# Kernel tuning notes

Measured on AMD Instinct MI355X. Metric: run time of the kernel, lower is better.

The kernel has to match this reference:

```python
import jax, jax.numpy as jnp
import numpy as np

B, C, H, W = 8, 512, 32, 32


def setup_inputs() -> dict:
    key = jax.random.key(0)
    ks = jax.random.split(key, 7)
    s = 0.02  # typical conv init scale
    return {
        "x": jax.random.normal(ks[0], (B, C, H, W), dtype=jnp.float32),
        "Wq": jax.random.normal(ks[1], (C, C), dtype=jnp.float32) * s,
        "bq": jax.random.normal(ks[2], (C,), dtype=jnp.float32) * s,
        "Wk": jax.random.normal(ks[3], (C, C), dtype=jnp.float32) * s,
        "bk": jax.random.normal(ks[4], (C,), dtype=jnp.float32) * s,
        "W6": jax.random.normal(ks[5], (C, C), dtype=jnp.float32) * s,
        "b6": jax.random.normal(ks[6], (C,), dtype=jnp.float32) * s,
    }


def _gam(x, Wq, bq, Wk, bk, W6, b6):
    b, c, h, w = x.shape
    hw = h * w
    scale = 1.0 / (c ** 0.5)
    # 1x1 convs == per-pixel channel matmuls (torch conv weight [out,in,1,1])
    q = jnp.einsum('bchw,dc->bhwd', x, Wq) + bq          # [B,H,W,C]
    q = q.reshape(b * hw, c)                              # query rows
    k = jnp.einsum('bchw,dc->bdhw', x, Wk) + bk[None, :, None, None]
    k = jnp.transpose(k, (1, 0, 2, 3)).reshape(c, b * hw)  # [C, B*HW]
    xw = (q.astype(jnp.float32) @ k.astype(jnp.float32))   # [B*HW, B*HW]
    xw = xw.reshape(b * hw, b, hw)
    xw = jnp.max(xw, axis=-1)                              # max over keys' spatial dim
    xw = jnp.mean(xw, axis=-1)                             # mean over key images
    xw = xw.reshape(b, hw) * scale
    xw = jax.nn.softmax(xw, axis=-1).astype(x.dtype)
    xw = xw.reshape(b, 1, h, w)
    x5 = x * xw
    return jnp.einsum('bchw,dc->bdhw', x5, W6) + b6[None, :, None, None]


def reference(x, Wq, bq, Wk, bk, W6, b6):
    x_new = _gam(x, Wq, bq, Wk, bk, W6, b6)
    # prototype: mean over batch and spatial dims, keep channels
    x_proto = jnp.mean(x_new.astype(jnp.float32), axis=(0, 2, 3)).astype(x.dtype)
    return x * x_proto[None, :, None, None]
```

## Files before the change

### kernel.cpp

```cpp
#include <hip/hip_runtime.h>
#include <hip/hip_bf16.h>

typedef __bf16 bf16_t;
typedef __bf16 bf16x8 __attribute__((ext_vector_type(8)));
typedef float f32x4 __attribute__((ext_vector_type(4)));

#define B_   8
#define C_   512
#define HW_  1024
#define NPIX 8192

typedef __attribute__((address_space(3))) void lds_vp;
typedef const __attribute__((address_space(1))) void gbl_vp;
__device__ __forceinline__ void gload_lds16(const void* g, void* l) {
    __builtin_amdgcn_global_load_lds((gbl_vp*)g, (lds_vp*)l, 16, 0, 0);
}

__device__ __forceinline__ void stage128x64_swz(const bf16_t* __restrict__ g,
                                                bf16_t* lds, int tid) {
    int w64 = tid & ~63;
#pragma unroll
    for (int s = 0; s < 4; ++s) {
        int u = s * 256 + tid;
        int row = u >> 3;
        int kg = (u & 7) ^ (row & 7);
        const bf16_t* src = g + (size_t)row * 512 + kg * 8;
        gload_lds16((const void*)src, (void*)(lds + (size_t)(s * 256 + w64) * 8));
    }
}

__global__ void k_transpose(const float* __restrict__ x, bf16_t* __restrict__ xT,
                            const float* __restrict__ Wq, const float* __restrict__ Wk,
                            bf16_t* __restrict__ wq, bf16_t* __restrict__ wk) {
    __shared__ bf16_t tile[64 * 66];
    int p0 = blockIdx.x * 64, c0 = blockIdx.y * 64, b = blockIdx.z;
    int t = threadIdx.x;
    int widx = ((blockIdx.z * 8 + blockIdx.y) * 16 + blockIdx.x) * 256 + t;
    wq[widx] = (bf16_t)Wq[widx];
    wk[widx] = (bf16_t)Wk[widx];
#pragma unroll
    for (int s = 0; s < 16; ++s) {
        int u = s * 256 + t;
        int cr = u >> 6, pc = u & 63;
        tile[cr * 66 + pc] = (bf16_t)x[((size_t)(b * C_ + c0 + cr)) * HW_ + p0 + pc];
    }
    __syncthreads();
#pragma unroll
    for (int s = 0; s < 16; ++s) {
        int u = s * 256 + t;
        int pr = u >> 6, cc = u & 63;
        xT[((size_t)(b * HW_ + p0 + pr)) * C_ + c0 + cc] = tile[cc * 66 + pr];
    }
}

__launch_bounds__(256, 2)
__global__ void k_gemm_qk(const bf16_t* __restrict__ xT,
                          const bf16_t* __restrict__ wq, const bf16_t* __restrict__ wk,
                          const float* __restrict__ bq, const float* __restrict__ bk,
                          bf16_t* __restrict__ qo, bf16_t* __restrict__ ko) {
    __shared__ __align__(16) bf16_t As[128 * 64];
    __shared__ __align__(16) bf16_t Bs[128 * 64];
    int bid = blockIdx.x;
    int mtile = bid >> 3;
    int nt = bid & 7;
    const bf16_t* wsel = (nt < 4) ? wq : wk;
    const float*  bsel = (nt < 4) ? bq : bk;
    bf16_t*       osel = (nt < 4) ? qo : ko;
    int nb = (nt & 3) * 128;
    int i0 = mtile * 128;
    int tid = threadIdx.x;
    int lane = tid & 63, w = tid >> 6;
    int wr = w >> 1, wc = w & 1, lr = lane & 15, lg = lane >> 4;
    int kswz = (lg ^ (lr & 7)) << 4;

    f32x4 acc[4][4];
#pragma unroll
    for (int mi = 0; mi < 4; ++mi)
#pragma unroll
        for (int ni = 0; ni < 4; ++ni)
#pragma unroll
            for (int r = 0; r < 4; ++r) acc[mi][ni][r] = 0.f;

    for (int kt = 0; kt < 8; ++kt) {
        int k0 = kt * 64;
        stage128x64_swz(xT + (size_t)i0 * 512 + k0, As, tid);
        stage128x64_swz(wsel + (size_t)nb * 512 + k0, Bs, tid);
        asm volatile("s_waitcnt vmcnt(0)" ::: "memory");
        __builtin_amdgcn_s_barrier();
#pragma unroll
        for (int kk = 0; kk < 2; ++kk) {
            bf16x8 af[4], bfr[4];
#pragma unroll
            for (int mi = 0; mi < 4; ++mi)
                af[mi] = *(const bf16x8*)((const char*)As +
                    (wr * 64 + mi * 16 + lr) * 128 + (kswz ^ (kk * 64)));
#pragma unroll
            for (int ni = 0; ni < 4; ++ni)
                bfr[ni] = *(const bf16x8*)((const char*)Bs +
                    (wc * 64 + ni * 16 + lr) * 128 + (kswz ^ (kk * 64)));
#pragma unroll
            for (int mi = 0; mi < 4; ++mi)
#pragma unroll
                for (int ni = 0; ni < 4; ++ni)
                    acc[mi][ni] = __builtin_amdgcn_mfma_f32_16x16x32_bf16(
                        af[mi], bfr[ni], acc[mi][ni], 0, 0, 0);
        }
        __builtin_amdgcn_s_barrier();
    }
#pragma unroll
    for (int ni = 0; ni < 4; ++ni) {
        int col = nb + wc * 64 + ni * 16 + lr;
        float bias = bsel[col];
#pragma unroll
        for (int mi = 0; mi < 4; ++mi) {
            int rowb = i0 + wr * 64 + mi * 16 + lg * 4;
#pragma unroll
            for (int r = 0; r < 4; ++r)
                osel[(size_t)(rowb + r) * 512 + col] = (bf16_t)(acc[mi][ni][r] + bias);
        }
    }
}


#define STAGE_A(RH, D, T)                                                          \
    gload_lds16((const void*)(q + srcA + (size_t)((RH) * 128) * 512 +              \
                              ((T) & 7) * 64),                                     \
                (void*)(ldsb + (RH) * 32768 + (D) * 16384 + ldw));                 \
    gload_lds16((const void*)(q + srcA + (size_t)((RH) * 128 + 64) * 512 +         \
                              ((T) & 7) * 64),                                     \
                (void*)(ldsb + (RH) * 32768 + (D) * 16384 + 8192 + ldw));

#define STAGE_B(RH, D, T)                                                          \
    gload_lds16((const void*)(kb + srcB +                                          \
                              (size_t)(((T) >> 3) * 256 + (RH) * 128) * 512 +      \
                              ((T) & 7) * 64),                                     \
                (void*)(ldsb + 65536 + (RH) * 32768 + (D) * 16384 + ldw));         \
    gload_lds16((const void*)(kb + srcB +                                          \
                              (size_t)(((T) >> 3) * 256 + (RH) * 128 + 64) * 512 + \
                              ((T) & 7) * 64),                                     \
                (void*)(ldsb + 65536 + (RH) * 32768 + (D) * 16384 + 8192 + ldw));

#define PHASE(D, KH, MH, STAGE_STMT, VM_STMT)                                      \
    {                                                                              \
        const char* Ab = ldsb + wr * 32768 + (D) * 16384;                          \
        const char* Bb = ldsb + 65536 + (wc >> 1) * 32768 + (D) * 16384;           \
        _Pragma("unroll")                                                          \
        for (int mi = 0; mi < 4; ++mi)                                             \
            af[mi] = *(const bf16x8*)(Ab + (aswz ^ ((KH) * 64)) +                  \
                                      ((MH) * 4 + mi) * 2048);                     \
        if ((MH) == 0) {                                                           \
            _Pragma("unroll")                                                      \
            for (int ni = 0; ni < 4; ++ni)                                         \
                bf[ni] = *(const bf16x8*)(Bb + (bswz ^ ((KH) * 64)) + ni * 2048);  \
        }                                                                          \
        STAGE_STMT;                                                                \
        __builtin_amdgcn_s_setprio(1);                                             \
        _Pragma("unroll")                                                          \
        for (int mi = 0; mi < 4; ++mi)                                             \
            _Pragma("unroll")                                                      \
            for (int ni = 0; ni < 4; ++ni)                                         \
                acc[(MH) * 4 + mi][ni] = __builtin_amdgcn_mfma_f32_16x16x32_bf16(  \
                    af[mi], bf[ni], acc[(MH) * 4 + mi][ni], 0, 0, 0);              \
        __builtin_amdgcn_s_setprio(0);                                             \
        VM_STMT;                                                                   \
        __builtin_amdgcn_s_barrier();                                              \
    }

__global__ __launch_bounds__(512, 2)
void k_gemm_max8(const bf16_t* __restrict__ q, const bf16_t* __restrict__ kp,
                 float* __restrict__ Mout) {
    __shared__ __align__(16) bf16_t lds[65536];
    char* ldsb = (char*)lds;
    int bid = blockIdx.x;
    int img = bid & 7;
    int qp = bid >> 3;
    int i0 = qp * 256;
    const bf16_t* kb = kp + (size_t)img * HW_ * C_;
    int tid = threadIdx.x;
    int lane = tid & 63, w = tid >> 6;
    int wr = w >> 2, wc = w & 3;
    int lr = lane & 15, lg = lane >> 4;
    int kswz = (lg ^ (lr & 7)) << 4;
    int aswz = lr * 128 + kswz;
    int bswz = ((wc & 1) * 64 + lr) * 128 + kswz;

    int srow = tid >> 3;
    int sk = (((tid & 7) ^ ((tid >> 3) & 7))) << 3;
    size_t srcA = (size_t)(i0 + srow) * 512 + sk;
    size_t srcB = (size_t)srow * 512 + sk;
    int ldw = (tid >> 6) * 1024;

    f32x4 acc[8][4];
    bf16x8 af[4], bf[4];
    float rm[8][4];
#pragma unroll
    for (int mi = 0; mi < 8; ++mi)
#pragma unroll
        for (int ni = 0; ni < 4; ++ni)
#pragma unroll
            for (int r = 0; r < 4; ++r) acc[mi][ni][r] = 0.f;
#pragma unroll
    for (int mi = 0; mi < 8; ++mi)
#pragma unroll
        for (int r = 0; r < 4; ++r) rm[mi][r] = -3.4e38f;

    STAGE_B(0, 0, 0) STAGE_A(0, 0, 0) STAGE_B(1, 0, 0) STAGE_A(1, 0, 0)
    STAGE_B(0, 1, 1)
    asm volatile("s_waitcnt vmcnt(2)" ::: "memory");
    __builtin_amdgcn_s_barrier();

    for (int i = 0; i < 16; ++i) {
        int tb = 2 * i + 1, tc = 2 * i + 2, td = 2 * i + 3;
        bool s = (i < 15);
        PHASE(0, 0, 0, { STAGE_A(0, 1, tb) }, {})
        PHASE(0, 0, 1, { STAGE_B(1, 1, tb) }, {})
        PHASE(0, 1, 0, { STAGE_A(1, 1, tb) }, {})
        PHASE(0, 1, 1, { if (s) { STAGE_B(0, 0, tc) } },
              { if (s) { asm volatile("s_waitcnt vmcnt(2)" ::: "memory"); }
                else   { asm volatile("s_waitcnt vmcnt(0)" ::: "memory"); } })
        PHASE(1, 0, 0, { if (s) { STAGE_A(0, 0, tc) } }, {})
        PHASE(1, 0, 1, { if (s) { STAGE_B(1, 0, tc) } }, {})
        PHASE(1, 1, 0, { if (s) { STAGE_A(1, 0, tc) } }, {})
        PHASE(1, 1, 1, { if (s) { STAGE_B(0, 1, td) } },
              { if (s) { asm volatile("s_waitcnt vmcnt(2)" ::: "memory"); } })
        if ((i & 3) == 3) {
#pragma unroll
            for (int mi = 0; mi < 8; ++mi)
#pragma unroll
                for (int r = 0; r < 4; ++r) {
                    float v = fmaxf(fmaxf(acc[mi][0][r], acc[mi][1][r]),
                                    fmaxf(acc[mi][2][r], acc[mi][3][r]));
                    rm[mi][r] = fmaxf(rm[mi][r], v);
#pragma unroll
                    for (int ni = 0; ni < 4; ++ni) acc[mi][ni][r] = 0.f;
                }
        }
    }

#pragma unroll
    for (int mi = 0; mi < 8; ++mi)
#pragma unroll
        for (int r = 0; r < 4; ++r) {
            float v = rm[mi][r];
#pragma unroll
            for (int off = 1; off < 16; off <<= 1) v = fmaxf(v, __shfl_xor(v, off));
            rm[mi][r] = v;
        }
    float* sm = (float*)lds;
    if (lr == 0) {
#pragma unroll
        for (int mi = 0; mi < 8; ++mi)
#pragma unroll
            for (int r = 0; r < 4; ++r)
                sm[wc * 256 + wr * 128 + mi * 16 + lg * 4 + r] = rm[mi][r];
    }
    __syncthreads();
    if (tid < 256) {
        float v = fmaxf(fmaxf(sm[tid], sm[256 + tid]),
                        fmaxf(sm[512 + tid], sm[768 + tid]));
        Mout[(size_t)(i0 + tid) * 8 + img] = v;
    }
}

__global__ void k_softmax(const float* __restrict__ Mout, float* __restrict__ wsm) {
    int b = blockIdx.x;
    int t = threadIdx.x;
    __shared__ float red[16];
    const float scale = 0.044194173824159216f;
    float s[4];
#pragma unroll
    for (int i = 0; i < 4; ++i) {
        int p = t + i * 256;
        const float* row = &Mout[(size_t)(b * 1024 + p) * 8];
        float acc = 0.f;
#pragma unroll
        for (int j = 0; j < 8; ++j) acc += row[j];
        s[i] = acc * (scale / 8.0f);
    }
    float m = fmaxf(fmaxf(s[0], s[1]), fmaxf(s[2], s[3]));
#pragma unroll
    for (int off = 1; off < 64; off <<= 1) m = fmaxf(m, __shfl_xor(m, off));
    if ((t & 63) == 0) red[t >> 6] = m;
    __syncthreads();
    float m4 = fmaxf(fmaxf(red[0], red[1]), fmaxf(red[2], red[3]));
    float e[4], sum = 0.f;
#pragma unroll
    for (int i = 0; i < 4; ++i) { e[i] = __expf(s[i] - m4); sum += e[i]; }
#pragma unroll
    for (int off = 1; off < 64; off <<= 1) sum += __shfl_xor(sum, off);
    if ((t & 63) == 0) red[8 + (t >> 6)] = sum;
    __syncthreads();
    float tot = red[8] + red[9] + red[10] + red[11];
    float inv = 1.0f / tot;
#pragma unroll
    for (int i = 0; i < 4; ++i) wsm[b * 1024 + t + i * 256] = e[i] * inv;
}

__global__ void k_reduce_y(const float* __restrict__ x, const float* __restrict__ wsm,
                           float* __restrict__ y) {
    int c = blockIdx.x;
    int t = threadIdx.x;
    float acc = 0.f;
    for (int b = 0; b < 8; ++b) {
        const float* xb = x + ((size_t)(b * C_ + c)) * HW_;
        const float* wb = wsm + b * HW_;
#pragma unroll
        for (int i = 0; i < 4; ++i) {
            int p = t + i * 256;
            acc += xb[p] * wb[p];
        }
    }
#pragma unroll
    for (int off = 1; off < 64; off <<= 1) acc += __shfl_xor(acc, off);
    __shared__ float red[4];
    if ((t & 63) == 0) red[t >> 6] = acc;
    __syncthreads();
    if (t == 0) y[c] = (red[0] + red[1] + red[2] + red[3]) * (1.0f / 8192.0f);
}

__global__ void k_proto(const float* __restrict__ W6, const float* __restrict__ b6,
                        const float* __restrict__ y, float* __restrict__ proto) {
    int d = blockIdx.x;
    int lane = threadIdx.x;
    float acc = 0.f;
#pragma unroll
    for (int i = 0; i < 8; ++i)
        acc += W6[(size_t)d * C_ + lane + i * 64] * y[lane + i * 64];
#pragma unroll
    for (int off = 1; off < 64; off <<= 1) acc += __shfl_xor(acc, off);
    if (lane == 0) proto[d] = acc + b6[d];
}

__global__ void k_final(const float* __restrict__ x, const float* __restrict__ proto,
                        float* __restrict__ out) {
    int idx = blockIdx.x * 256 + threadIdx.x;
    float4 v = ((const float4*)x)[idx];
    int c = (idx >> 8) & 511;
    float p = proto[c];
    v.x *= p; v.y *= p; v.z *= p; v.w *= p;
    ((float4*)out)[idx] = v;
}

extern "C" void kernel_launch(void* const* d_in, const int* in_sizes, int n_in,
                              void* d_out, int out_size, void* d_ws, size_t ws_size,
                              hipStream_t stream) {
    const float* x  = (const float*)d_in[0];
    const float* Wq = (const float*)d_in[1];
    const float* bq = (const float*)d_in[2];
    const float* Wk = (const float*)d_in[3];
    const float* bk = (const float*)d_in[4];
    const float* W6 = (const float*)d_in[5];
    const float* b6 = (const float*)d_in[6];
    float* out = (float*)d_out;

    char* ws = (char*)d_ws;
    bf16_t* xT    = (bf16_t*)(ws);
    float*  Mout  = (float*)(ws);
    bf16_t* wqb   = (bf16_t*)(ws + 8388608);
    bf16_t* wkb   = (bf16_t*)(ws + 8912896);
    bf16_t* qb    = (bf16_t*)(ws + 9437184);
    bf16_t* kb    = (bf16_t*)(ws + 17825792);
    float*  wsm   = (float*)(ws + 26476544);
    float*  yv    = (float*)(ws + 26509312);
    float*  proto = (float*)(ws + 26511360);

    hipLaunchKernelGGL(k_transpose, dim3(16, 8, 8), dim3(256), 0, stream,
                       x, xT, Wq, Wk, wqb, wkb);
    hipLaunchKernelGGL(k_gemm_qk, dim3(512), dim3(256), 0, stream,
                       xT, wqb, wkb, bq, bk, qb, kb);
    hipLaunchKernelGGL(k_gemm_max8, dim3(256), dim3(512), 0, stream, qb, kb, Mout);
    hipLaunchKernelGGL(k_softmax, dim3(8), dim3(256), 0, stream, Mout, wsm);
    hipLaunchKernelGGL(k_reduce_y, dim3(512), dim3(256), 0, stream, x, wsm, yv);
    hipLaunchKernelGGL(k_proto, dim3(512), dim3(64), 0, stream, W6, b6, yv, proto);
    hipLaunchKernelGGL(k_final, dim3(4096), dim3(256), 0, stream, x, proto, out);
}
```

Measured before the change: 96.13 us.

## Vectorize transpose and reductions, fuse proto matvec into final scaling kernel

Vectorizes the x transpose loads and xT stores to float4/bf16x4 and changes the LDS padding. It also uses float4 loads in softmax and reduce_y. The separate k_proto launch is removed: each k_final block now recomputes its channel's dot product of a W6 row with y before scaling x. This saves one launch and improves memory coalescing, at the cost of recomputing the matvec 8 times per channel, and the padding change may introduce LDS bank conflicts.

```diff
diff --git a/kernel.cpp b/kernel.cpp
--- a/kernel.cpp
+++ b/kernel.cpp
@@ -3,6 +3,7 @@
 
 typedef __bf16 bf16_t;
 typedef __bf16 bf16x8 __attribute__((ext_vector_type(8)));
+typedef __bf16 bf16x4 __attribute__((ext_vector_type(4)));
 typedef float f32x4 __attribute__((ext_vector_type(4)));
 
 #define B_   8
@@ -32,24 +33,33 @@
 __global__ void k_transpose(const float* __restrict__ x, bf16_t* __restrict__ xT,
                             const float* __restrict__ Wq, const float* __restrict__ Wk,
                             bf16_t* __restrict__ wq, bf16_t* __restrict__ wk) {
-    __shared__ bf16_t tile[64 * 66];
+    __shared__ bf16_t tile[64 * 65];
     int p0 = blockIdx.x * 64, c0 = blockIdx.y * 64, b = blockIdx.z;
     int t = threadIdx.x;
     int widx = ((blockIdx.z * 8 + blockIdx.y) * 16 + blockIdx.x) * 256 + t;
     wq[widx] = (bf16_t)Wq[widx];
     wk[widx] = (bf16_t)Wk[widx];
 #pragma unroll
-    for (int s = 0; s < 16; ++s) {
+    for (int s = 0; s < 4; ++s) {
         int u = s * 256 + t;
-        int cr = u >> 6, pc = u & 63;
-        tile[cr * 66 + pc] = (bf16_t)x[((size_t)(b * C_ + c0 + cr)) * HW_ + p0 + pc];
-    }
-    __syncthreads();
-#pragma unroll
-    for (int s = 0; s < 16; ++s) {
+        int cr = u >> 4, pc = (u & 15) * 4;
+        float4 v = *(const float4*)&x[((size_t)(b * C_ + c0 + cr)) * HW_ + p0 + pc];
+        tile[cr * 65 + pc + 0] = (bf16_t)v.x;
+        tile[cr * 65 + pc + 1] = (bf16_t)v.y;
+        tile[cr * 65 + pc + 2] = (bf16_t)v.z;
+        tile[cr * 65 + pc + 3] = (bf16_t)v.w;
+    }
+    __syncthreads();
+#pragma unroll
+    for (int s = 0; s < 4; ++s) {
         int u = s * 256 + t;
-        int pr = u >> 6, cc = u & 63;
-        xT[((size_t)(b * HW_ + p0 + pr)) * C_ + c0 + cc] = tile[cc * 66 + pr];
+        int pr = u >> 4, cc = (u & 15) * 4;
+        bf16x4 o;
+        o[0] = tile[(cc + 0) * 65 + pr];
+        o[1] = tile[(cc + 1) * 65 + pr];
+        o[2] = tile[(cc + 2) * 65 + pr];
+        o[3] = tile[(cc + 3) * 65 + pr];
+        *(bf16x4*)&xT[((size_t)(b * HW_ + p0 + pr)) * C_ + c0 + cc] = o;
     }
 }
 
@@ -271,10 +281,9 @@
 #pragma unroll
     for (int i = 0; i < 4; ++i) {
         int p = t + i * 256;
-        const float* row = &Mout[(size_t)(b * 1024 + p) * 8];
-        float acc = 0.f;
-#pragma unroll
-        for (int j = 0; j < 8; ++j) acc += row[j];
+        const float4* row = (const float4*)&Mout[(size_t)(b * 1024 + p) * 8];
+        float4 r0 = row[0], r1 = row[1];
+        float acc = (r0.x + r0.y + r0.z + r0.w) + (r1.x + r1.y + r1.z + r1.w);
         s[i] = acc * (scale / 8.0f);
     }
     float m = fmaxf(fmaxf(s[0], s[1]), fmaxf(s[2], s[3]));
@@ -301,14 +310,11 @@
     int c = blockIdx.x;
     int t = threadIdx.x;
     float acc = 0.f;
+#pragma unroll
     for (int b = 0; b < 8; ++b) {
-        const float* xb = x + ((size_t)(b * C_ + c)) * HW_;
-        const float* wb = wsm + b * HW_;
-#pragma unroll
-        for (int i = 0; i < 4; ++i) {
-            int p = t + i * 256;
-            acc += xb[p] * wb[p];
-        }
+        float4 xv = ((const float4*)(x + ((size_t)(b * C_ + c)) * HW_))[t];
+        float4 wv = ((const float4*)(wsm + b * HW_))[t];
+        acc += xv.x * wv.x + xv.y * wv.y + xv.z * wv.z + xv.w * wv.w;
     }
 #pragma unroll
     for (int off = 1; off < 64; off <<= 1) acc += __shfl_xor(acc, off);
@@ -318,25 +324,22 @@
     if (t == 0) y[c] = (red[0] + red[1] + red[2] + red[3]) * (1.0f / 8192.0f);
 }
 
-__global__ void k_proto(const float* __restrict__ W6, const float* __restrict__ b6,
-                        const float* __restrict__ y, float* __restrict__ proto) {
-    int d = blockIdx.x;
-    int lane = threadIdx.x;
-    float acc = 0.f;
-#pragma unroll
-    for (int i = 0; i < 8; ++i)
-        acc += W6[(size_t)d * C_ + lane + i * 64] * y[lane + i * 64];
-#pragma unroll
-    for (int off = 1; off < 64; off <<= 1) acc += __shfl_xor(acc, off);
-    if (lane == 0) proto[d] = acc + b6[d];
-}
-
-__global__ void k_final(const float* __restrict__ x, const float* __restrict__ proto,
+__global__ void k_final(const float* __restrict__ x, const float* __restrict__ W6,
+                        const float* __restrict__ b6, const float* __restrict__ y,
                         float* __restrict__ out) {
-    int idx = blockIdx.x * 256 + threadIdx.x;
+    int bid = blockIdx.x;
+    int t = threadIdx.x;
+    int c = bid & 511;
+    float a = W6[(size_t)c * C_ + t] * y[t] +
+              W6[(size_t)c * C_ + t + 256] * y[t + 256];
+#pragma unroll
+    for (int off = 1; off < 64; off <<= 1) a += __shfl_xor(a, off);
+    __shared__ float red[4];
+    if ((t & 63) == 0) red[t >> 6] = a;
+    __syncthreads();
+    float p = red[0] + red[1] + red[2] + red[3] + b6[c];
+    int idx = bid * 256 + t;
     float4 v = ((const float4*)x)[idx];
-    int c = (idx >> 8) & 511;
-    float p = proto[c];
     v.x *= p; v.y *= p; v.z *= p; v.w *= p;
     ((float4*)out)[idx] = v;
 }
@@ -362,7 +365,6 @@
     bf16_t* kb    = (bf16_t*)(ws + 17825792);
     float*  wsm   = (float*)(ws + 26476544);
     float*  yv    = (float*)(ws + 26509312);
-    float*  proto = (float*)(ws + 26511360);
 
     hipLaunchKernelGGL(k_transpose, dim3(16, 8, 8), dim3(256), 0, stream,
                        x, xT, Wq, Wk, wqb, wkb);
@@ -371,6 +373,5 @@
     hipLaunchKernelGGL(k_gemm_max8, dim3(256), dim3(512), 0, stream, qb, kb, Mout);
     hipLaunchKernelGGL(k_softmax, dim3(8), dim3(256), 0, stream, Mout, wsm);
     hipLaunchKernelGGL(k_reduce_y, dim3(512), dim3(256), 0, stream, x, wsm, yv);
-    hipLaunchKernelGGL(k_proto, dim3(512), dim3(64), 0, stream, W6, b6, yv, proto);
-    hipLaunchKernelGGL(k_final, dim3(4096), dim3(256), 0, stream, x, proto, out);
-}
+    hipLaunchKernelGGL(k_final, dim3(4096), dim3(256), 0, stream, x, W6, b6, yv, out);
+}
```

After: 95.16 us. Within noise of the previous version (-1.0%).
